# Optimization experiments

Hardware: AMD Instinct MI355X
Metric: run time of the kernel (lower is better)

The kernel has to match this reference:

```python
import jax, jax.numpy as jnp
import numpy as np

NUM_LAYERS = 12
D = 256          # d_model
H = 8            # n_head
DK = D // H      # qk_dim = v_dim = 32
FFD = 1024       # ffd_dim
B, L = 32, 448
EPS = 1e-6
MAXLEN = 500


def _sinusoidal_pos_emb(maxlen, hidden_dim):
    depth = hidden_dim / 2
    positions = np.arange(maxlen, dtype=np.float32)[:, None]
    depths = np.arange(depth, dtype=np.float32)[None, :] / depth
    angle_rads = positions * (1.0 / np.power(10000.0, depths))
    pe = np.concatenate([np.sin(angle_rads), np.cos(angle_rads)], axis=-1)
    return jnp.asarray(pe, jnp.float32)


def setup_inputs() -> dict:
    key = jax.random.key(0)
    ks = jax.random.split(key, 16)
    s = 0.02
    inp = {
        "x": jax.random.normal(ks[0], (B, L, D), jnp.float32),
        "mask": jnp.zeros((B, L), jnp.bool_),
        "pos_emb": _sinusoidal_pos_emb(MAXLEN - 1, D)[:L],  # [L, D]
        "Wq": jax.random.normal(ks[1], (NUM_LAYERS, D, D), jnp.float32) * s,
        "bq": jnp.zeros((NUM_LAYERS, D), jnp.float32),
        "Wk": jax.random.normal(ks[2], (NUM_LAYERS, D, D), jnp.float32) * s,
        "bk": jnp.zeros((NUM_LAYERS, D), jnp.float32),
        "Wv": jax.random.normal(ks[3], (NUM_LAYERS, D, D), jnp.float32) * s,
        "bv": jnp.zeros((NUM_LAYERS, D), jnp.float32),
        "Wo": jax.random.normal(ks[4], (NUM_LAYERS, D, D), jnp.float32) * s,
        "bo": jnp.zeros((NUM_LAYERS, D), jnp.float32),
        "W1": jax.random.normal(ks[5], (NUM_LAYERS, D, FFD), jnp.float32) * s,
        "bf1": jnp.zeros((NUM_LAYERS, FFD), jnp.float32),
        "W2": jax.random.normal(ks[6], (NUM_LAYERS, FFD, D), jnp.float32) * s,
        "bf2": jnp.zeros((NUM_LAYERS, D), jnp.float32),
        "ln1_g": jnp.ones((NUM_LAYERS, D), jnp.float32),
        "ln1_b": jnp.zeros((NUM_LAYERS, D), jnp.float32),
        "ln2_g": jnp.ones((NUM_LAYERS, D), jnp.float32),
        "ln2_b": jnp.zeros((NUM_LAYERS, D), jnp.float32),
    }
    return inp


def _layer_norm(x, g, b):
    mu = jnp.mean(x, axis=-1, keepdims=True)
    var = jnp.mean(jnp.square(x - mu), axis=-1, keepdims=True)
    return (x - mu) * jax.lax.rsqrt(var + EPS) * g + b


def _encoder_forward(x, mask, pos_emb, Wq, bq, Wk, bk, Wv, bv, Wo, bo,
                     W1, bf1, W2, bf2, ln1_g, ln1_b, ln2_g, ln2_b):
    Bx, Lx, _ = x.shape
    scale = 1.0 / np.sqrt(DK)
    x = x + pos_emb[None, :Lx, :]
    mask_b = mask[:, None, None, :]  # [B,1,1,L], True = masked
    for i in range(NUM_LAYERS):
        # --- pre-norm attention ---
        nx = _layer_norm(x, ln1_g[i], ln1_b[i])
        q = (nx @ Wq[i] + bq[i]).reshape(Bx, Lx, H, DK)
        k = (nx @ Wk[i] + bk[i]).reshape(Bx, Lx, H, DK)
        v = (nx @ Wv[i] + bv[i]).reshape(Bx, Lx, H, DK)
        dot = jnp.einsum("bihd,bjhd->bhij", q, k) * scale
        dot = jnp.where(mask_b, -10000.0, dot)
        attn = jax.nn.softmax(dot, axis=-1)
        o = jnp.einsum("bhij,bjhd->bihd", attn, v).reshape(Bx, Lx, D)
        x = x + (o @ Wo[i] + bo[i])
        # --- pre-norm FFN (exact GELU, as torch nn.GELU) ---
        nx2 = _layer_norm(x, ln2_g[i], ln2_b[i])
        h = jax.nn.gelu(nx2 @ W1[i] + bf1[i], approximate=False)
        x = x + (h @ W2[i] + bf2[i])
    return x


def reference(x, mask, pos_emb, Wq, bq, Wk, bk, Wv, bv, Wo, bo,
              W1, bf1, W2, bf2, ln1_g, ln1_b, ln2_g, ln2_b):
    return _encoder_forward(x, mask, pos_emb, Wq, bq, Wk, bk, Wv, bv, Wo, bo,
                            W1, bf1, W2, bf2, ln1_g, ln1_b, ln2_g, ln2_b)
```

## Files before the change

### kernel.cpp

```cpp
#include <hip/hip_runtime.h>

#define NL 12
#define DM 256
#define FFDIM 1024
#define BBATCH 32
#define LSEQ 448
#define MTOK (BBATCH*LSEQ)
#define EPSF 1e-6f

typedef __attribute__((ext_vector_type(8))) short bf16x8;
typedef __attribute__((ext_vector_type(4))) float f32x4;
typedef unsigned short u16;
typedef unsigned int u32;

__device__ __forceinline__ u16 f2bf(float f) {
    union { float f; u32 u; } v; v.f = f;
    u32 r = v.u + 0x7fffu + ((v.u >> 16) & 1u);
    return (u16)(r >> 16);
}
__device__ __forceinline__ float gelu_exact(float x) {
    return 0.5f * x * (1.0f + erff(x * 0.70710678118654752f));
}
__device__ __forceinline__ void gload16(const u16* g, u16* l) {
    __builtin_amdgcn_global_load_lds(
        (const __attribute__((address_space(1))) u32*)g,
        (__attribute__((address_space(3))) u32*)l, 16, 0, 0);
}

__global__ __launch_bounds__(256) void add_pos_k(
    const float* __restrict__ x, const float* __restrict__ pe, float* __restrict__ out)
{
    int i = blockIdx.x * 256 + threadIdx.x;
    float4 xv = ((const float4*)x)[i];
    float4 pv = ((const float4*)pe)[i % (LSEQ * DM / 4)];
    float4 r;
    r.x = xv.x + pv.x; r.y = xv.y + pv.y; r.z = xv.z + pv.z; r.w = xv.w + pv.w;
    ((float4*)out)[i] = r;
}

__global__ __launch_bounds__(256) void ln_k(
    const float* __restrict__ x, const float* __restrict__ g,
    const float* __restrict__ b, u16* __restrict__ out)
{
    const int w = threadIdx.x >> 6, lane = threadIdx.x & 63;
    const int row = blockIdx.x * 4 + w;
    float4 v = ((const float4*)(x + (size_t)row * DM))[lane];
    float s = v.x + v.y + v.z + v.w;
#pragma unroll
    for (int off = 32; off; off >>= 1) s += __shfl_xor(s, off);
    float mu = s * (1.0f / 256.0f);
    float d0 = v.x - mu, d1 = v.y - mu, d2 = v.z - mu, d3 = v.w - mu;
    float sq = d0*d0 + d1*d1 + d2*d2 + d3*d3;
#pragma unroll
    for (int off = 32; off; off >>= 1) sq += __shfl_xor(sq, off);
    float rs = rsqrtf(sq * (1.0f / 256.0f) + EPSF);
    float4 gv = ((const float4*)g)[lane];
    float4 bv = ((const float4*)b)[lane];
    ushort4 o;
    o.x = f2bf(d0 * rs * gv.x + bv.x);
    o.y = f2bf(d1 * rs * gv.y + bv.y);
    o.z = f2bf(d2 * rs * gv.z + bv.z);
    o.w = f2bf(d3 * rs * gv.w + bv.w);
    *(ushort4*)(out + (size_t)row * DM + lane * 4) = o;
}

__global__ __launch_bounds__(256) void twt_k(
    const float* __restrict__ in, u16* __restrict__ out,
    int K, int N, int in_lstride, int out_lstride)
{
    __shared__ float tl[32][33];
    const int l = blockIdx.z;
    const int n0 = blockIdx.x * 32, k0 = blockIdx.y * 32;
    const int tx = threadIdx.x & 31, ty = threadIdx.x >> 5;
    const float* src = in + (size_t)l * in_lstride;
#pragma unroll
    for (int i = 0; i < 4; ++i)
        tl[ty + 8*i][tx] = src[(size_t)(k0 + ty + 8*i) * N + n0 + tx];
    __syncthreads();
    u16* dst = out + (size_t)l * out_lstride;
#pragma unroll
    for (int i = 0; i < 4; ++i)
        dst[(size_t)(n0 + ty + 8*i) * K + k0 + tx] = f2bf(tl[tx][ty + 8*i]);
}

__global__ __launch_bounds__(256) void pack_bias_k(
    const float* __restrict__ bq, const float* __restrict__ bk,
    const float* __restrict__ bv, float* __restrict__ bqkv)
{
    int i = blockIdx.x * 256 + threadIdx.x;
    if (i >= NL * 768) return;
    int l = i / 768, c = i % 768;
    float v = (c < 256) ? bq[l*256 + c] : (c < 512) ? bk[l*256 + c - 256] : bv[l*256 + c - 512];
    bqkv[i] = v;
}

__global__ __launch_bounds__(256) void vt_k(
    const u16* __restrict__ qkv, u16* __restrict__ vtg)
{
    __shared__ u16 tl[32][33];
    const int kt = blockIdx.x, h = blockIdx.y, b = blockIdx.z;
    const int tx = threadIdx.x & 31, ty = threadIdx.x >> 5;
#pragma unroll
    for (int i = 0; i < 4; ++i)
        tl[ty + 8*i][tx] = qkv[(size_t)(b*LSEQ + kt*32 + ty + 8*i) * 768 + 512 + h*32 + tx];
    __syncthreads();
#pragma unroll
    for (int i = 0; i < 4; ++i)
        vtg[((size_t)(b*8 + h)*32 + ty + 8*i) * 448 + kt*32 + tx] = tl[tx][ty + 8*i];
}

template<int BN, int EPI>
__global__ __launch_bounds__(256, 2) void mm_k(
    const u16* __restrict__ A, int lda, const u16* __restrict__ Bt,
    const float* __restrict__ bias, void* __restrict__ C, int ldc, int K)
{
    __shared__ u16 As[2 * 128 * 32];
    __shared__ u16 Bs[2 * BN * 32];
    constexpr int MT = (BN == 128) ? 4 : 2;
    constexpr int BPANEL = BN * 32;
    const int tid = threadIdx.x;
    const int by = blockIdx.x, bx = blockIdx.y;
    const int w = tid >> 6, lane = tid & 63;
    const int lm = lane & 15, lk = lane >> 4;
    const int wm = (BN == 128) ? (w >> 1) : w;
    const int wn = (BN == 128) ? (w & 1) : 0;
    const int m0 = wm * MT * 16;
    const int n0 = wn * 64;
    const int lrow = lane >> 2, lcol = (lane & 3) * 8;

    const u16* Ab = A + (size_t)(by * 128) * lda;
    const u16* Bb = Bt + (size_t)(bx * BN) * K;

    f32x4 zz = {0.f, 0.f, 0.f, 0.f};
    f32x4 acc[MT][4];
#pragma unroll
    for (int i = 0; i < MT; ++i)
#pragma unroll
        for (int j = 0; j < 4; ++j) acc[i][j] = zz;

    for (int k0 = 0; k0 < K; k0 += 64) {
        __syncthreads();
#pragma unroll
        for (int p = 0; p < 2; ++p) {
#pragma unroll
            for (int i = 0; i < 2; ++i) {
                int seg = w * 2 + i;
                gload16(Ab + (size_t)(seg * 16 + lrow) * lda + k0 + p * 32 + lcol,
                        &As[p * 4096 + seg * 512]);
            }
            if constexpr (BN == 128) {
#pragma unroll
                for (int i = 0; i < 2; ++i) {
                    int seg = w * 2 + i;
                    gload16(Bb + (size_t)(seg * 16 + lrow) * K + k0 + p * 32 + lcol,
                            &Bs[p * BPANEL + seg * 512]);
                }
            } else {
                gload16(Bb + (size_t)(w * 16 + lrow) * K + k0 + p * 32 + lcol,
                        &Bs[p * BPANEL + w * 512]);
            }
        }
        __syncthreads();

#pragma unroll
        for (int p = 0; p < 2; ++p) {
            bf16x8 af[MT], bfr[4];
#pragma unroll
            for (int mt = 0; mt < MT; ++mt)
                af[mt] = *(const bf16x8*)&As[p * 4096 + (m0 + mt*16 + lm)*32 + lk*8];
#pragma unroll
            for (int nt = 0; nt < 4; ++nt)
                bfr[nt] = *(const bf16x8*)&Bs[p * BPANEL + (n0 + nt*16 + lm)*32 + lk*8];
#pragma unroll
            for (int mt = 0; mt < MT; ++mt)
#pragma unroll
                for (int nt = 0; nt < 4; ++nt)
                    acc[mt][nt] = __builtin_amdgcn_mfma_f32_16x16x32_bf16(af[mt], bfr[nt], acc[mt][nt], 0, 0, 0);
        }
    }

    float bv[4];
#pragma unroll
    for (int nt = 0; nt < 4; ++nt) bv[nt] = bias[bx*BN + n0 + nt*16 + lm];
#pragma unroll
    for (int mt = 0; mt < MT; ++mt) {
#pragma unroll
        for (int r = 0; r < 4; ++r) {
            int grow = by*128 + m0 + mt*16 + lk*4 + r;
#pragma unroll
            for (int nt = 0; nt < 4; ++nt) {
                int gcol = bx*BN + n0 + nt*16 + lm;
                float vv = acc[mt][nt][r] + bv[nt];
                if constexpr (EPI == 0) {
                    ((u16*)C)[(size_t)grow * ldc + gcol] = f2bf(vv);
                } else if constexpr (EPI == 1) {
                    ((u16*)C)[(size_t)grow * ldc + gcol] = f2bf(gelu_exact(vv));
                } else {
                    float* p = (float*)C + (size_t)grow * ldc + gcol;
                    *p += vv;
                }
            }
        }
    }
}

__global__ __launch_bounds__(256, 2) void attn_k(
    const u16* __restrict__ qkv, const u16* __restrict__ vtg,
    const unsigned char* __restrict__ mask, u16* __restrict__ ob)
{
    __shared__ u16 Klds[448 * 32];
    __shared__ u16 Plds[4][16 * 68];
    const int tid = threadIdx.x, w = tid >> 6, lane = tid & 63;
    const int lm = lane & 15, lk = lane >> 4;
    const int bid = blockIdx.x;
    const int bh = bid & 255, sg = bid >> 8;
    const int b = bh >> 3, h = bh & 7;
    const size_t rowbase = (size_t)b * LSEQ;

#pragma unroll
    for (int i = 0; i < 7; ++i) {
        int seg = w * 7 + i;
        gload16(qkv + (rowbase + seg * 16 + (lane >> 2)) * 768 + 256 + h * 32 + (lane & 3) * 8,
                &Klds[seg * 512]);
    }
    unsigned mbits = 0;
#pragma unroll
    for (int t = 0; t < 28; ++t)
        mbits |= (mask[b * LSEQ + t * 16 + lm] ? 1u : 0u) << t;
    __syncthreads();

    const u16* Vb = vtg + (size_t)bh * 32 * 448;
    const float scale = 0.17677669529663687f;
    f32x4 zz = {0.f, 0.f, 0.f, 0.f};

    const int q0 = (sg * 4 + w) * 16;
    bf16x8 qf = *(const bf16x8*)(qkv + (rowbase + q0 + lm) * 768 + h * 32 + lk * 8);
    f32x4 sc[28];
#pragma unroll
    for (int t = 0; t < 28; ++t) {
        bf16x8 kf = *(const bf16x8*)&Klds[(t*16 + lm)*32 + lk*8];
        sc[t] = __builtin_amdgcn_mfma_f32_16x16x32_bf16(qf, kf, zz, 0, 0, 0);
    }
    float mx[4] = {-1e30f, -1e30f, -1e30f, -1e30f};
#pragma unroll
    for (int t = 0; t < 28; ++t) {
        bool m = (mbits >> t) & 1;
#pragma unroll
        for (int r = 0; r < 4; ++r) {
            float v = m ? -10000.0f : sc[t][r] * scale;
            sc[t][r] = v;
            mx[r] = fmaxf(mx[r], v);
        }
    }
#pragma unroll
    for (int off = 1; off < 16; off <<= 1)
#pragma unroll
        for (int r = 0; r < 4; ++r) mx[r] = fmaxf(mx[r], __shfl_xor(mx[r], off));
    float sum[4] = {0.f, 0.f, 0.f, 0.f};
#pragma unroll
    for (int t = 0; t < 28; ++t)
#pragma unroll
        for (int r = 0; r < 4; ++r) {
            float e = __expf(sc[t][r] - mx[r]);
            sc[t][r] = e;
            sum[r] += e;
        }
#pragma unroll
    for (int off = 1; off < 16; off <<= 1)
#pragma unroll
        for (int r = 0; r < 4; ++r) sum[r] += __shfl_xor(sum[r], off);
    float inv[4];
#pragma unroll
    for (int r = 0; r < 4; ++r) inv[r] = 1.0f / sum[r];

    f32x4 oacc[2] = {zz, zz};
    u16* P = &Plds[w][0];
#pragma unroll
    for (int cc = 0; cc < 7; ++cc) {
#pragma unroll
        for (int tt = 0; tt < 4; ++tt) {
            int t = cc*4 + tt;
#pragma unroll
            for (int r = 0; r < 4; ++r)
                P[(lk*4 + r)*68 + tt*16 + lm] = f2bf(sc[t][r]);
        }
        bf16x8 pa0 = *(const bf16x8*)&P[lm*68 + lk*8];
        bf16x8 pa1 = *(const bf16x8*)&P[lm*68 + 32 + lk*8];
#pragma unroll
        for (int dt = 0; dt < 2; ++dt) {
            bf16x8 vb0 = *(const bf16x8*)(Vb + (size_t)(dt*16 + lm)*448 + cc*64 + lk*8);
            bf16x8 vb1 = *(const bf16x8*)(Vb + (size_t)(dt*16 + lm)*448 + cc*64 + 32 + lk*8);
            oacc[dt] = __builtin_amdgcn_mfma_f32_16x16x32_bf16(pa0, vb0, oacc[dt], 0, 0, 0);
            oacc[dt] = __builtin_amdgcn_mfma_f32_16x16x32_bf16(pa1, vb1, oacc[dt], 0, 0, 0);
        }
    }
#pragma unroll
    for (int dt = 0; dt < 2; ++dt)
#pragma unroll
        for (int r = 0; r < 4; ++r)
            ob[(rowbase + q0 + lk*4 + r)*256 + h*32 + dt*16 + lm] = f2bf(oacc[dt][r] * inv[r]);
}

extern "C" void kernel_launch(void* const* d_in, const int* in_sizes, int n_in,
                              void* d_out, int out_size, void* d_ws, size_t ws_size,
                              hipStream_t stream)
{
    const float* x_in = (const float*)d_in[0];
    const unsigned char* mask = (const unsigned char*)d_in[1];
    const float* pe   = (const float*)d_in[2];
    const float* Wq = (const float*)d_in[3];
    const float* bq = (const float*)d_in[4];
    const float* Wk = (const float*)d_in[5];
    const float* bk = (const float*)d_in[6];
    const float* Wv = (const float*)d_in[7];
    const float* bv = (const float*)d_in[8];
    const float* Wo = (const float*)d_in[9];
    const float* bo = (const float*)d_in[10];
    const float* W1 = (const float*)d_in[11];
    const float* bf1 = (const float*)d_in[12];
    const float* W2 = (const float*)d_in[13];
    const float* bf2 = (const float*)d_in[14];
    const float* ln1_g = (const float*)d_in[15];
    const float* ln1_b = (const float*)d_in[16];
    const float* ln2_g = (const float*)d_in[17];
    const float* ln2_b = (const float*)d_in[18];

    float* x = (float*)d_out;
    u16* ws = (u16*)d_ws;
    u16* nx   = ws;
    u16* qkv  = nx + 3670016;
    u16* ob   = qkv + 11010048;
    u16* vtg  = ob + 3670016;
    u16* hb   = qkv;
    u16* wqkvt = vtg + 3670016;
    u16* wot  = wqkvt + 2359296;
    u16* w1t  = wot + 786432;
    u16* w2t  = w1t + 3145728;
    float* bqkv = (float*)(w2t + 3145728);

    add_pos_k<<<MTOK * DM / 1024, 256, 0, stream>>>(x_in, pe, x);

    twt_k<<<dim3(8, 8, NL), 256, 0, stream>>>(Wq, wqkvt,          256, 256, 65536, 196608);
    twt_k<<<dim3(8, 8, NL), 256, 0, stream>>>(Wk, wqkvt + 65536,  256, 256, 65536, 196608);
    twt_k<<<dim3(8, 8, NL), 256, 0, stream>>>(Wv, wqkvt + 131072, 256, 256, 65536, 196608);
    twt_k<<<dim3(8, 8, NL), 256, 0, stream>>>(Wo, wot, 256, 256, 65536, 65536);
    twt_k<<<dim3(32, 8, NL), 256, 0, stream>>>(W1, w1t, 256, 1024, 262144, 262144);
    twt_k<<<dim3(8, 32, NL), 256, 0, stream>>>(W2, w2t, 1024, 256, 262144, 262144);
    pack_bias_k<<<(NL * 768 + 255) / 256, 256, 0, stream>>>(bq, bk, bv, bqkv);

    for (int l = 0; l < NL; ++l) {
        ln_k<<<MTOK / 4, 256, 0, stream>>>(x, ln1_g + l*256, ln1_b + l*256, nx);
        mm_k<128, 0><<<dim3(112, 6), 256, 0, stream>>>(
            nx, 256, wqkvt + (size_t)l*196608, bqkv + l*768, qkv, 768, 256);
        vt_k<<<dim3(14, 8, 32), 256, 0, stream>>>(qkv, vtg);
        attn_k<<<1792, 256, 0, stream>>>(qkv, vtg, mask, ob);
        mm_k<64, 2><<<dim3(112, 4), 256, 0, stream>>>(
            ob, 256, wot + (size_t)l*65536, bo + l*256, x, 256, 256);
        ln_k<<<MTOK / 4, 256, 0, stream>>>(x, ln2_g + l*256, ln2_b + l*256, nx);
        mm_k<128, 1><<<dim3(112, 8), 256, 0, stream>>>(
            nx, 256, w1t + (size_t)l*262144, bf1 + l*1024, hb, 1024, 256);
        mm_k<64, 2><<<dim3(112, 4), 256, 0, stream>>>(
            hb, 1024, w2t + (size_t)l*262144, bf2 + l*256, x, 256, 1024);
    }
}
```

Baseline: 1.563 ms.

## Fuse layernorm into GEMMs, V transpose into QKV epilogue, streamline attention softmax

LayerNorm is now computed inside the QKV and FFN1 GEMM kernels, writing the normalized 128-row tile straight into shared memory. This removes the separate ln_k launches and the bf16 nx round trip. The QKV epilogue writes V directly in transposed layout, which drops vt_k, and folds the softmax scale and log2e into Q. Attention skips max subtraction and computes exp2 scores on the fly, so the 28-tile score array no longer sits in registers. This risks overflow if logits are large, and it raises launch-bound occupancy. The costs are redundant LN recomputation across the N-tiles and narrower 64-column tiles for the GEMMs.

Measured after the change: 2.979 ms. 90.6% more time.

```diff
diff --git a/kernel.cpp b/kernel.cpp
--- a/kernel.cpp
+++ b/kernel.cpp
@@ -7,6 +7,7 @@
 #define LSEQ 448
 #define MTOK (BBATCH*LSEQ)
 #define EPSF 1e-6f
+#define QSCALE_LOG2E (0.17677669529663687f * 1.4426950408889634f)
 
 typedef __attribute__((ext_vector_type(8))) short bf16x8;
 typedef __attribute__((ext_vector_type(4))) float f32x4;
@@ -38,32 +39,6 @@
     ((float4*)out)[i] = r;
 }
 
-__global__ __launch_bounds__(256) void ln_k(
-    const float* __restrict__ x, const float* __restrict__ g,
-    const float* __restrict__ b, u16* __restrict__ out)
-{
-    const int w = threadIdx.x >> 6, lane = threadIdx.x & 63;
-    const int row = blockIdx.x * 4 + w;
-    float4 v = ((const float4*)(x + (size_t)row * DM))[lane];
-    float s = v.x + v.y + v.z + v.w;
-#pragma unroll
-    for (int off = 32; off; off >>= 1) s += __shfl_xor(s, off);
-    float mu = s * (1.0f / 256.0f);
-    float d0 = v.x - mu, d1 = v.y - mu, d2 = v.z - mu, d3 = v.w - mu;
-    float sq = d0*d0 + d1*d1 + d2*d2 + d3*d3;
-#pragma unroll
-    for (int off = 32; off; off >>= 1) sq += __shfl_xor(sq, off);
-    float rs = rsqrtf(sq * (1.0f / 256.0f) + EPSF);
-    float4 gv = ((const float4*)g)[lane];
-    float4 bv = ((const float4*)b)[lane];
-    ushort4 o;
-    o.x = f2bf(d0 * rs * gv.x + bv.x);
-    o.y = f2bf(d1 * rs * gv.y + bv.y);
-    o.z = f2bf(d2 * rs * gv.z + bv.z);
-    o.w = f2bf(d3 * rs * gv.w + bv.w);
-    *(ushort4*)(out + (size_t)row * DM + lane * 4) = o;
-}
-
 __global__ __launch_bounds__(256) void twt_k(
     const float* __restrict__ in, u16* __restrict__ out,
     int K, int N, int in_lstride, int out_lstride)
@@ -94,47 +69,136 @@
     bqkv[i] = v;
 }
 
-__global__ __launch_bounds__(256) void vt_k(
-    const u16* __restrict__ qkv, u16* __restrict__ vtg)
-{
-    __shared__ u16 tl[32][33];
-    const int kt = blockIdx.x, h = blockIdx.y, b = blockIdx.z;
-    const int tx = threadIdx.x & 31, ty = threadIdx.x >> 5;
-#pragma unroll
-    for (int i = 0; i < 4; ++i)
-        tl[ty + 8*i][tx] = qkv[(size_t)(b*LSEQ + kt*32 + ty + 8*i) * 768 + 512 + h*32 + tx];
-    __syncthreads();
-#pragma unroll
-    for (int i = 0; i < 4; ++i)
-        vtg[((size_t)(b*8 + h)*32 + ty + 8*i) * 448 + kt*32 + tx] = tl[tx][ty + 8*i];
-}
-
-template<int BN, int EPI>
-__global__ __launch_bounds__(256, 2) void mm_k(
-    const u16* __restrict__ A, int lda, const u16* __restrict__ Bt,
-    const float* __restrict__ bias, void* __restrict__ C, int ldc, int K)
-{
-    __shared__ u16 As[2 * 128 * 32];
-    __shared__ u16 Bs[2 * BN * 32];
-    constexpr int MT = (BN == 128) ? 4 : 2;
-    constexpr int BPANEL = BN * 32;
+template<int EPI>
+__global__ __launch_bounds__(256, 2) void mmln_k(
+    const float* __restrict__ X, const float* __restrict__ g,
+    const float* __restrict__ b, const u16* __restrict__ Bt,
+    const float* __restrict__ bias, u16* __restrict__ C, int ldc,
+    u16* __restrict__ vtg)
+{
+    __shared__ u16 As[128 * 264];
+    __shared__ u16 Bs[2][64 * 32];
     const int tid = threadIdx.x;
     const int by = blockIdx.x, bx = blockIdx.y;
     const int w = tid >> 6, lane = tid & 63;
     const int lm = lane & 15, lk = lane >> 4;
-    const int wm = (BN == 128) ? (w >> 1) : w;
-    const int wn = (BN == 128) ? (w & 1) : 0;
-    const int m0 = wm * MT * 16;
-    const int n0 = wn * 64;
+    const int m0 = w * 32;
     const int lrow = lane >> 2, lcol = (lane & 3) * 8;
 
+    float4 gv4 = ((const float4*)g)[lane];
+    float4 bv4 = ((const float4*)b)[lane];
+    for (int i = 0; i < 32; ++i) {
+        int row = m0 + i;
+        float4 xv = *(const float4*)(X + (size_t)(by * 128 + row) * 256 + lane * 4);
+        float s = xv.x + xv.y + xv.z + xv.w;
+#pragma unroll
+        for (int off = 32; off; off >>= 1) s += __shfl_xor(s, off);
+        float mu = s * (1.0f / 256.0f);
+        float d0 = xv.x - mu, d1 = xv.y - mu, d2 = xv.z - mu, d3 = xv.w - mu;
+        float sq = d0*d0 + d1*d1 + d2*d2 + d3*d3;
+#pragma unroll
+        for (int off = 32; off; off >>= 1) sq += __shfl_xor(sq, off);
+        float rs = rsqrtf(sq * (1.0f / 256.0f) + EPSF);
+        ushort4 o;
+        o.x = f2bf(d0 * rs * gv4.x + bv4.x);
+        o.y = f2bf(d1 * rs * gv4.y + bv4.y);
+        o.z = f2bf(d2 * rs * gv4.z + bv4.z);
+        o.w = f2bf(d3 * rs * gv4.w + bv4.w);
+        *(ushort4*)&As[row * 264 + lane * 4] = o;
+    }
+
+    const u16* Bb = Bt + (size_t)(bx * 64) * 256;
+    f32x4 zz = {0.f, 0.f, 0.f, 0.f};
+    f32x4 acc[2][4];
+#pragma unroll
+    for (int i = 0; i < 2; ++i)
+#pragma unroll
+        for (int j = 0; j < 4; ++j) acc[i][j] = zz;
+
+    for (int k0 = 0; k0 < 256; k0 += 64) {
+        __syncthreads();
+        gload16(Bb + (size_t)(w * 16 + lrow) * 256 + k0 + lcol,      &Bs[0][w * 512]);
+        gload16(Bb + (size_t)(w * 16 + lrow) * 256 + k0 + 32 + lcol, &Bs[1][w * 512]);
+        __syncthreads();
+#pragma unroll
+        for (int p = 0; p < 2; ++p) {
+            bf16x8 af[2], bfr[4];
+#pragma unroll
+            for (int mt = 0; mt < 2; ++mt)
+                af[mt] = *(const bf16x8*)&As[(m0 + mt*16 + lm) * 264 + k0 + p*32 + lk*8];
+#pragma unroll
+            for (int nt = 0; nt < 4; ++nt)
+                bfr[nt] = *(const bf16x8*)&Bs[p][(nt*16 + lm) * 32 + lk*8];
+#pragma unroll
+            for (int mt = 0; mt < 2; ++mt)
+#pragma unroll
+                for (int nt = 0; nt < 4; ++nt)
+                    acc[mt][nt] = __builtin_amdgcn_mfma_f32_16x16x32_bf16(af[mt], bfr[nt], acc[mt][nt], 0, 0, 0);
+        }
+    }
+
+    float bv[4];
+#pragma unroll
+    for (int nt = 0; nt < 4; ++nt) bv[nt] = bias[bx*64 + nt*16 + lm];
+#pragma unroll
+    for (int mt = 0; mt < 2; ++mt) {
+        int grow0 = by*128 + m0 + mt*16 + lk*4;
+#pragma unroll
+        for (int nt = 0; nt < 4; ++nt) {
+            int gcol = bx*64 + nt*16 + lm;
+            float v0 = acc[mt][nt][0] + bv[nt];
+            float v1 = acc[mt][nt][1] + bv[nt];
+            float v2 = acc[mt][nt][2] + bv[nt];
+            float v3 = acc[mt][nt][3] + bv[nt];
+            if constexpr (EPI == 1) {
+                u16* cp = C + (size_t)grow0 * ldc + gcol;
+                cp[0]       = f2bf(gelu_exact(v0));
+                cp[ldc]     = f2bf(gelu_exact(v1));
+                cp[2*ldc]   = f2bf(gelu_exact(v2));
+                cp[3*ldc]   = f2bf(gelu_exact(v3));
+            } else {
+                if (gcol < 512) {
+                    float qs = (gcol < 256) ? QSCALE_LOG2E : 1.0f;
+                    u16* cp = C + (size_t)grow0 * ldc + gcol;
+                    cp[0]     = f2bf(v0 * qs);
+                    cp[ldc]   = f2bf(v1 * qs);
+                    cp[2*ldc] = f2bf(v2 * qs);
+                    cp[3*ldc] = f2bf(v3 * qs);
+                } else {
+                    int c = gcol - 512;
+                    int hh = c >> 5, d = c & 31;
+                    u32 bidx = (u32)grow0 / 448u;
+                    int srow = grow0 - (int)bidx * 448;
+                    ushort4 st;
+                    st.x = f2bf(v0); st.y = f2bf(v1); st.z = f2bf(v2); st.w = f2bf(v3);
+                    *(ushort4*)&vtg[((size_t)(bidx*8 + hh)*32 + d)*448 + srow] = st;
+                }
+            }
+        }
+    }
+}
+
+template<int EPI>
+__global__ __launch_bounds__(256, 4) void mm_k(
+    const u16* __restrict__ A, int lda, const u16* __restrict__ Bt,
+    const float* __restrict__ bias, void* __restrict__ C, int ldc, int K)
+{
+    __shared__ u16 As[2 * 128 * 32];
+    __shared__ u16 Bs[2 * 64 * 32];
+    const int tid = threadIdx.x;
+    const int by = blockIdx.x, bx = blockIdx.y;
+    const int w = tid >> 6, lane = tid & 63;
+    const int lm = lane & 15, lk = lane >> 4;
+    const int m0 = w * 32;
+    const int lrow = lane >> 2, lcol = (lane & 3) * 8;
+
     const u16* Ab = A + (size_t)(by * 128) * lda;
-    const u16* Bb = Bt + (size_t)(bx * BN) * K;
+    const u16* Bb = Bt + (size_t)(bx * 64) * K;
 
     f32x4 zz = {0.f, 0.f, 0.f, 0.f};
-    f32x4 acc[MT][4];
-#pragma unroll
-    for (int i = 0; i < MT; ++i)
+    f32x4 acc[2][4];
+#pragma unroll
+    for (int i = 0; i < 2; ++i)
 #pragma unroll
         for (int j = 0; j < 4; ++j) acc[i][j] = zz;
 
@@ -148,31 +212,21 @@
                 gload16(Ab + (size_t)(seg * 16 + lrow) * lda + k0 + p * 32 + lcol,
                         &As[p * 4096 + seg * 512]);
             }
-            if constexpr (BN == 128) {
-#pragma unroll
-                for (int i = 0; i < 2; ++i) {
-                    int seg = w * 2 + i;
-                    gload16(Bb + (size_t)(seg * 16 + lrow) * K + k0 + p * 32 + lcol,
-                            &Bs[p * BPANEL + seg * 512]);
-                }
-            } else {
-                gload16(Bb + (size_t)(w * 16 + lrow) * K + k0 + p * 32 + lcol,
-                        &Bs[p * BPANEL + w * 512]);
-            }
+            gload16(Bb + (size_t)(w * 16 + lrow) * K + k0 + p * 32 + lcol,
+                    &Bs[p * 2048 + w * 512]);
         }
         __syncthreads();
-
 #pragma unroll
         for (int p = 0; p < 2; ++p) {
-            bf16x8 af[MT], bfr[4];
-#pragma unroll
-            for (int mt = 0; mt < MT; ++mt)
+            bf16x8 af[2], bfr[4];
+#pragma unroll
+            for (int mt = 0; mt < 2; ++mt)
                 af[mt] = *(const bf16x8*)&As[p * 4096 + (m0 + mt*16 + lm)*32 + lk*8];
 #pragma unroll
             for (int nt = 0; nt < 4; ++nt)
-                bfr[nt] = *(const bf16x8*)&Bs[p * BPANEL + (n0 + nt*16 + lm)*32 + lk*8];
-#pragma unroll
-            for (int mt = 0; mt < MT; ++mt)
+                bfr[nt] = *(const bf16x8*)&Bs[p * 2048 + (nt*16 + lm)*32 + lk*8];
+#pragma unroll
+            for (int mt = 0; mt < 2; ++mt)
 #pragma unroll
                 for (int nt = 0; nt < 4; ++nt)
                     acc[mt][nt] = __builtin_amdgcn_mfma_f32_16x16x32_bf16(af[mt], bfr[nt], acc[mt][nt], 0, 0, 0);
@@ -181,30 +235,24 @@
 
     float bv[4];
 #pragma unroll
-    for (int nt = 0; nt < 4; ++nt) bv[nt] = bias[bx*BN + n0 + nt*16 + lm];
-#pragma unroll
-    for (int mt = 0; mt < MT; ++mt) {
+    for (int nt = 0; nt < 4; ++nt) bv[nt] = bias[bx*64 + nt*16 + lm];
+#pragma unroll
+    for (int mt = 0; mt < 2; ++mt) {
 #pragma unroll
         for (int r = 0; r < 4; ++r) {
             int grow = by*128 + m0 + mt*16 + lk*4 + r;
 #pragma unroll
             for (int nt = 0; nt < 4; ++nt) {
-                int gcol = bx*BN + n0 + nt*16 + lm;
+                int gcol = bx*64 + nt*16 + lm;
                 float vv = acc[mt][nt][r] + bv[nt];
-                if constexpr (EPI == 0) {
-                    ((u16*)C)[(size_t)grow * ldc + gcol] = f2bf(vv);
-                } else if constexpr (EPI == 1) {
-                    ((u16*)C)[(size_t)grow * ldc + gcol] = f2bf(gelu_exact(vv));
-                } else {
-                    float* p = (float*)C + (size_t)grow * ldc + gcol;
-                    *p += vv;
-                }
+                float* p = (float*)C + (size_t)grow * ldc + gcol;
+                *p += vv;
             }
         }
     }
 }
 
-__global__ __launch_bounds__(256, 2) void attn_k(
+__global__ __launch_bounds__(256, 4) void attn_k(
     const u16* __restrict__ qkv, const u16* __restrict__ vtg,
     const unsigned char* __restrict__ mask, u16* __restrict__ ob)
 {
@@ -230,59 +278,28 @@
     __syncthreads();
 
     const u16* Vb = vtg + (size_t)bh * 32 * 448;
-    const float scale = 0.17677669529663687f;
     f32x4 zz = {0.f, 0.f, 0.f, 0.f};
 
     const int q0 = (sg * 4 + w) * 16;
     bf16x8 qf = *(const bf16x8*)(qkv + (rowbase + q0 + lm) * 768 + h * 32 + lk * 8);
-    f32x4 sc[28];
-#pragma unroll
-    for (int t = 0; t < 28; ++t) {
-        bf16x8 kf = *(const bf16x8*)&Klds[(t*16 + lm)*32 + lk*8];
-        sc[t] = __builtin_amdgcn_mfma_f32_16x16x32_bf16(qf, kf, zz, 0, 0, 0);
-    }
-    float mx[4] = {-1e30f, -1e30f, -1e30f, -1e30f};
-#pragma unroll
-    for (int t = 0; t < 28; ++t) {
-        bool m = (mbits >> t) & 1;
-#pragma unroll
-        for (int r = 0; r < 4; ++r) {
-            float v = m ? -10000.0f : sc[t][r] * scale;
-            sc[t][r] = v;
-            mx[r] = fmaxf(mx[r], v);
-        }
-    }
-#pragma unroll
-    for (int off = 1; off < 16; off <<= 1)
-#pragma unroll
-        for (int r = 0; r < 4; ++r) mx[r] = fmaxf(mx[r], __shfl_xor(mx[r], off));
+
+    f32x4 oacc[2] = {zz, zz};
     float sum[4] = {0.f, 0.f, 0.f, 0.f};
-#pragma unroll
-    for (int t = 0; t < 28; ++t)
-#pragma unroll
-        for (int r = 0; r < 4; ++r) {
-            float e = __expf(sc[t][r] - mx[r]);
-            sc[t][r] = e;
-            sum[r] += e;
-        }
-#pragma unroll
-    for (int off = 1; off < 16; off <<= 1)
-#pragma unroll
-        for (int r = 0; r < 4; ++r) sum[r] += __shfl_xor(sum[r], off);
-    float inv[4];
-#pragma unroll
-    for (int r = 0; r < 4; ++r) inv[r] = 1.0f / sum[r];
-
-    f32x4 oacc[2] = {zz, zz};
     u16* P = &Plds[w][0];
 #pragma unroll
     for (int cc = 0; cc < 7; ++cc) {
 #pragma unroll
         for (int tt = 0; tt < 4; ++tt) {
             int t = cc*4 + tt;
-#pragma unroll
-            for (int r = 0; r < 4; ++r)
-                P[(lk*4 + r)*68 + tt*16 + lm] = f2bf(sc[t][r]);
+            bf16x8 kf = *(const bf16x8*)&Klds[(t*16 + lm)*32 + lk*8];
+            f32x4 s = __builtin_amdgcn_mfma_f32_16x16x32_bf16(qf, kf, zz, 0, 0, 0);
+            bool m = (mbits >> t) & 1;
+#pragma unroll
+            for (int r = 0; r < 4; ++r) {
+                float e = m ? 0.f : exp2f(s[r]);
+                sum[r] += e;
+                P[(lk*4 + r)*68 + tt*16 + lm] = f2bf(e);
+            }
         }
         bf16x8 pa0 = *(const bf16x8*)&P[lm*68 + lk*8];
         bf16x8 pa1 = *(const bf16x8*)&P[lm*68 + 32 + lk*8];
@@ -294,6 +311,14 @@
             oacc[dt] = __builtin_amdgcn_mfma_f32_16x16x32_bf16(pa1, vb1, oacc[dt], 0, 0, 0);
         }
     }
+#pragma unroll
+    for (int off = 1; off < 16; off <<= 1)
+#pragma unroll
+        for (int r = 0; r < 4; ++r) sum[r] += __shfl_xor(sum[r], off);
+    float inv[4];
+#pragma unroll
+    for (int r = 0; r < 4; ++r) inv[r] = 1.0f / sum[r];
+
 #pragma unroll
     for (int dt = 0; dt < 2; ++dt)
 #pragma unroll
@@ -327,8 +352,7 @@
 
     float* x = (float*)d_out;
     u16* ws = (u16*)d_ws;
-    u16* nx   = ws;
-    u16* qkv  = nx + 3670016;
+    u16* qkv  = ws;
     u16* ob   = qkv + 11010048;
     u16* vtg  = ob + 3670016;
     u16* hb   = qkv;
@@ -349,17 +373,16 @@
     pack_bias_k<<<(NL * 768 + 255) / 256, 256, 0, stream>>>(bq, bk, bv, bqkv);
 
     for (int l = 0; l < NL; ++l) {
-        ln_k<<<MTOK / 4, 256, 0, stream>>>(x, ln1_g + l*256, ln1_b + l*256, nx);
-        mm_k<128, 0><<<dim3(112, 6), 256, 0, stream>>>(
-            nx, 256, wqkvt + (size_t)l*196608, bqkv + l*768, qkv, 768, 256);
-        vt_k<<<dim3(14, 8, 32), 256, 0, stream>>>(qkv, vtg);
+        mmln_k<0><<<dim3(112, 12), 256, 0, stream>>>(
+            x, ln1_g + l*256, ln1_b + l*256, wqkvt + (size_t)l*196608,
+            bqkv + l*768, qkv, 768, vtg);
         attn_k<<<1792, 256, 0, stream>>>(qkv, vtg, mask, ob);
-        mm_k<64, 2><<<dim3(112, 4), 256, 0, stream>>>(
+        mm_k<2><<<dim3(112, 4), 256, 0, stream>>>(
             ob, 256, wot + (size_t)l*65536, bo + l*256, x, 256, 256);
-        ln_k<<<MTOK / 4, 256, 0, stream>>>(x, ln2_g + l*256, ln2_b + l*256, nx);
-        mm_k<128, 1><<<dim3(112, 8), 256, 0, stream>>>(
-            nx, 256, w1t + (size_t)l*262144, bf1 + l*1024, hb, 1024, 256);
-        mm_k<64, 2><<<dim3(112, 4), 256, 0, stream>>>(
+        mmln_k<1><<<dim3(112, 16), 256, 0, stream>>>(
+            x, ln2_g + l*256, ln2_b + l*256, w1t + (size_t)l*262144,
+            bf1 + l*1024, hb, 1024, nullptr);
+        mm_k<2><<<dim3(112, 4), 256, 0, stream>>>(
             hb, 1024, w2t + (size_t)l*262144, bf2 + l*256, x, 256, 1024);
     }
 }
```
